# Optimization experiments

Hardware: AMD Instinct MI355X
Metric: run time of the kernel (lower is better)

Reference implementation:

```python
import jax, jax.numpy as jnp
import numpy as np

K_TOKENS = 40  # safety_token_count
LN_EPS = 1e-5


def setup_inputs() -> dict:
    key = jax.random.key(0)
    ks = jax.random.split(key, 3)
    B, S, D = 16, 4096, 768
    H = D // 2
    features = jax.random.normal(ks[0], (B, S, D), dtype=jnp.float32)
    W1 = jax.random.normal(ks[1], (D, H), dtype=jnp.float32) * (1.0 / np.sqrt(D))
    b1 = jnp.zeros((H,), dtype=jnp.float32)
    ln_gamma = jnp.ones((H,), dtype=jnp.float32)
    ln_beta = jnp.zeros((H,), dtype=jnp.float32)
    W2 = jax.random.normal(ks[2], (H, 1), dtype=jnp.float32) * (1.0 / np.sqrt(H))
    b2 = jnp.zeros((1,), dtype=jnp.float32)
    return {"features": features, "W1": W1, "b1": b1,
            "ln_gamma": ln_gamma, "ln_beta": ln_beta, "W2": W2, "b2": b2}


def _scores(features, W1, b1, ln_gamma, ln_beta, W2, b2):
    # Linear -> LayerNorm -> GELU(exact) -> Dropout(eval=identity) -> Linear -> Sigmoid
    h = jnp.einsum('bsd,dh->bsh', features, W1) + b1
    mu = jnp.mean(h, axis=-1, keepdims=True)
    var = jnp.mean(jnp.square(h - mu), axis=-1, keepdims=True)
    h = (h - mu) * jax.lax.rsqrt(var + LN_EPS) * ln_gamma + ln_beta
    h = jax.nn.gelu(h, approximate=False)
    s = jnp.einsum('bsh,ho->bso', h, W2) + b2  # [B, S, 1]
    return jax.nn.sigmoid(s[..., 0])           # [B, S]


def reference(features, W1, b1, ln_gamma, ln_beta, W2, b2):
    scores = _scores(features, W1, b1, ln_gamma, ln_beta, W2, b2)
    k = min(K_TOKENS, features.shape[1])
    _, indices = jax.lax.top_k(scores, k)                      # [B, k]
    safety_tokens = jnp.take_along_axis(features, indices[:, :, None], axis=1)  # [B, k, D]
    return safety_tokens, indices
```

## Files before the change

### kernel.cpp

```cpp
#include <hip/hip_runtime.h>
#include <math.h>

#define B_   16
#define S_   4096
#define D_   768
#define H_   384
#define NTOK (B_ * S_)
#define KTOP 40
#define NTILES 24
#define KCH    24

typedef __attribute__((ext_vector_type(8))) short bf16x8;
typedef __attribute__((ext_vector_type(4))) float f32x4;

static __device__ __forceinline__ unsigned short f2bf(float x) {
    union { float f; unsigned u; } v; v.f = x;
    unsigned r = v.u + 0x7FFF + ((v.u >> 16) & 1);
    return (unsigned short)(r >> 16);
}
static __device__ __forceinline__ float bf2f(unsigned short h) {
    union { unsigned u; float f; } v; v.u = ((unsigned)h) << 16; return v.f;
}

__global__ __launch_bounds__(64) void pack_w1(const float* __restrict__ W1,
                                              unsigned short* __restrict__ bh,
                                              unsigned short* __restrict__ bl)
{
    const int nt   = blockIdx.x;
    const int ch   = blockIdx.y;
    const int lane = threadIdx.x;
    const int n    = nt * 16 + (lane & 15);
    const int k0   = ch * 32 + (lane >> 4) * 8;

    unsigned short h8[8], l8[8];
#pragma unroll
    for (int j = 0; j < 8; ++j) {
        const float v = W1[(size_t)(k0 + j) * H_ + n];
        const unsigned short h = f2bf(v);
        h8[j] = h;
        l8[j] = f2bf(v - bf2f(h));
    }
    const size_t base = ((size_t)(nt * KCH + ch) * 64 + lane) * 8;
#pragma unroll
    for (int j = 0; j < 8; ++j) { bh[base + j] = h8[j]; bl[base + j] = l8[j]; }
}

__global__ __launch_bounds__(256) void score_kernel(
    const float* __restrict__ features,
    const unsigned short* __restrict__ bh_g,
    const unsigned short* __restrict__ bl_g,
    const float* __restrict__ b1,
    const float* __restrict__ gamma,
    const float* __restrict__ beta,
    const float* __restrict__ W2,
    const float* __restrict__ b2,
    float* __restrict__ scores)
{
    __shared__ unsigned short Ah[64][40];
    __shared__ unsigned short Al[64][40];
    __shared__ float red[4][64];
    __shared__ float mu_s[64];
    __shared__ float rs_s[64];

    const int tid  = threadIdx.x;
    const int lane = tid & 63;
    const int w    = tid >> 6;
    const int base = blockIdx.x * 64;
    const int cl   = lane & 15;
    const int p    = lane >> 4;

    f32x4 acc[4][6];
#pragma unroll
    for (int m = 0; m < 4; ++m)
#pragma unroll
        for (int t = 0; t < 6; ++t) acc[m][t] = (f32x4){0.f, 0.f, 0.f, 0.f};

    const int f0 = tid, f1 = tid + 256;
    const int r0 = f0 >> 3, c0 = (f0 & 7) * 4;
    const int r1 = f1 >> 3, c1 = (f1 & 7) * 4;

    float4 p0 = *(const float4*)(features + (size_t)(base + r0) * D_ + c0);
    float4 p1 = *(const float4*)(features + (size_t)(base + r1) * D_ + c1);

    for (int c = 0; c < KCH; ++c) {
        if (c) __syncthreads();
        {
            unsigned short h0 = f2bf(p0.x), h1 = f2bf(p0.y), h2 = f2bf(p0.z), h3 = f2bf(p0.w);
            Ah[r0][c0] = h0; Ah[r0][c0+1] = h1; Ah[r0][c0+2] = h2; Ah[r0][c0+3] = h3;
            Al[r0][c0]   = f2bf(p0.x - bf2f(h0));
            Al[r0][c0+1] = f2bf(p0.y - bf2f(h1));
            Al[r0][c0+2] = f2bf(p0.z - bf2f(h2));
            Al[r0][c0+3] = f2bf(p0.w - bf2f(h3));
            unsigned short g0 = f2bf(p1.x), g1 = f2bf(p1.y), g2 = f2bf(p1.z), g3 = f2bf(p1.w);
            Ah[r1][c1] = g0; Ah[r1][c1+1] = g1; Ah[r1][c1+2] = g2; Ah[r1][c1+3] = g3;
            Al[r1][c1]   = f2bf(p1.x - bf2f(g0));
            Al[r1][c1+1] = f2bf(p1.y - bf2f(g1));
            Al[r1][c1+2] = f2bf(p1.z - bf2f(g2));
            Al[r1][c1+3] = f2bf(p1.w - bf2f(g3));
        }
        if (c + 1 < KCH) {
            const int d0 = (c + 1) * 32;
            p0 = *(const float4*)(features + (size_t)(base + r0) * D_ + d0 + c0);
            p1 = *(const float4*)(features + (size_t)(base + r1) * D_ + d0 + c1);
        }
        __syncthreads();

        bf16x8 bhf[6], blf[6];
#pragma unroll
        for (int t = 0; t < 6; ++t) {
            const size_t bb = ((size_t)((w * 6 + t) * KCH + c) * 64 + lane) * 8;
            bhf[t] = *(const bf16x8*)(bh_g + bb);
            blf[t] = *(const bf16x8*)(bl_g + bb);
        }
        bf16x8 ahf[4], alf[4];
#pragma unroll
        for (int m = 0; m < 4; ++m) {
            const int row = m * 16 + cl;
            const int k0  = p * 8;
            ahf[m] = *(const bf16x8*)&Ah[row][k0];
            alf[m] = *(const bf16x8*)&Al[row][k0];
        }
#pragma unroll
        for (int m = 0; m < 4; ++m)
#pragma unroll
            for (int t = 0; t < 6; ++t) {
                acc[m][t] = __builtin_amdgcn_mfma_f32_16x16x32_bf16(ahf[m], bhf[t], acc[m][t], 0, 0, 0);
                acc[m][t] = __builtin_amdgcn_mfma_f32_16x16x32_bf16(ahf[m], blf[t], acc[m][t], 0, 0, 0);
                acc[m][t] = __builtin_amdgcn_mfma_f32_16x16x32_bf16(alf[m], bhf[t], acc[m][t], 0, 0, 0);
            }
    }

    float b1v[6], gv[6], bev[6], w2v[6];
#pragma unroll
    for (int t = 0; t < 6; ++t) {
        const int n = (w * 6 + t) * 16 + cl;
        b1v[t] = b1[n]; gv[t] = gamma[n]; bev[t] = beta[n]; w2v[t] = W2[n];
    }
#pragma unroll
    for (int m = 0; m < 4; ++m)
#pragma unroll
        for (int t = 0; t < 6; ++t)
#pragma unroll
            for (int r = 0; r < 4; ++r) acc[m][t][r] += b1v[t];

#pragma unroll
    for (int m = 0; m < 4; ++m) {
        float sm[4] = {0.f, 0.f, 0.f, 0.f};
#pragma unroll
        for (int t = 0; t < 6; ++t)
#pragma unroll
            for (int r = 0; r < 4; ++r) sm[r] += acc[m][t][r];
#pragma unroll
        for (int r = 0; r < 4; ++r) {
#pragma unroll
            for (int off = 1; off <= 8; off <<= 1) sm[r] += __shfl_xor(sm[r], off, 64);
        }
        if (cl == 0) {
#pragma unroll
            for (int r = 0; r < 4; ++r) red[w][m * 16 + p * 4 + r] = sm[r];
        }
    }
    __syncthreads();
    if (tid < 64) mu_s[tid] = (red[0][tid] + red[1][tid] + red[2][tid] + red[3][tid]) * (1.0f / H_);
    __syncthreads();

#pragma unroll
    for (int m = 0; m < 4; ++m) {
        float mur[4];
#pragma unroll
        for (int r = 0; r < 4; ++r) mur[r] = mu_s[m * 16 + p * 4 + r];
        float sm[4] = {0.f, 0.f, 0.f, 0.f};
#pragma unroll
        for (int t = 0; t < 6; ++t)
#pragma unroll
            for (int r = 0; r < 4; ++r) { const float d = acc[m][t][r] - mur[r]; sm[r] += d * d; }
#pragma unroll
        for (int r = 0; r < 4; ++r) {
#pragma unroll
            for (int off = 1; off <= 8; off <<= 1) sm[r] += __shfl_xor(sm[r], off, 64);
        }
        if (cl == 0) {
#pragma unroll
            for (int r = 0; r < 4; ++r) red[w][m * 16 + p * 4 + r] = sm[r];
        }
    }
    __syncthreads();
    if (tid < 64) rs_s[tid] = rsqrtf((red[0][tid] + red[1][tid] + red[2][tid] + red[3][tid]) * (1.0f / H_) + 1e-5f);
    __syncthreads();

#pragma unroll
    for (int m = 0; m < 4; ++m) {
        float mur[4], rsr[4];
#pragma unroll
        for (int r = 0; r < 4; ++r) { mur[r] = mu_s[m * 16 + p * 4 + r]; rsr[r] = rs_s[m * 16 + p * 4 + r]; }
        float sm[4] = {0.f, 0.f, 0.f, 0.f};
#pragma unroll
        for (int t = 0; t < 6; ++t)
#pragma unroll
            for (int r = 0; r < 4; ++r) {
                const float y  = (acc[m][t][r] - mur[r]) * rsr[r] * gv[t] + bev[t];
                const float ge = 0.5f * y * (1.0f + erff(y * 0.70710678118654752f));
                sm[r] = fmaf(ge, w2v[t], sm[r]);
            }
#pragma unroll
        for (int r = 0; r < 4; ++r) {
#pragma unroll
            for (int off = 1; off <= 8; off <<= 1) sm[r] += __shfl_xor(sm[r], off, 64);
        }
        if (cl == 0) {
#pragma unroll
            for (int r = 0; r < 4; ++r) red[w][m * 16 + p * 4 + r] = sm[r];
        }
    }
    __syncthreads();
    if (tid < 64) {
        const float s = red[0][tid] + red[1][tid] + red[2][tid] + red[3][tid] + b2[0];
        scores[base + tid] = 1.0f / (1.0f + expf(-s));
    }
}

__global__ __launch_bounds__(256) void select_kernel(const float* __restrict__ scores,
                                                     int* __restrict__ sel)
{
    __shared__ unsigned int bits_s[S_];
    __shared__ unsigned int hist[256];
    __shared__ int s_byte, s_above, s_rem;
    __shared__ unsigned int s_ngt, s_neq;
    __shared__ unsigned int candV[64];
    __shared__ int candI[64];
    __shared__ int eqI[256];

    const int b   = blockIdx.x;
    const int tid = threadIdx.x;

    for (int i = tid; i < S_; i += 256)
        bits_s[i] = __float_as_uint(scores[b * S_ + i]);
    if (tid == 0) { s_rem = KTOP; s_ngt = 0u; s_neq = 0u; }

    unsigned int prefix = 0u, mask = 0u;
    for (int pb = 3; pb >= 0; --pb) {
        hist[tid] = 0u;
        __syncthreads();
        for (int i = tid; i < S_; i += 256) {
            const unsigned int u = bits_s[i];
            if ((u & mask) == prefix) atomicAdd(&hist[(u >> (8 * pb)) & 255u], 1u);
        }
        __syncthreads();
        if (tid == 0) {
            int c = 0, v = 255;
            for (; v >= 0; --v) { c += (int)hist[v]; if (c >= s_rem) break; }
            s_byte  = v;
            s_above = c - (int)hist[v];
            s_rem   = s_rem - s_above;
        }
        __syncthreads();
        prefix |= ((unsigned int)s_byte) << (8 * pb);
        mask   |= 0xFFu << (8 * pb);
        __syncthreads();
    }
    const unsigned int T = prefix;
    const int need = s_rem;

    for (int i = tid; i < S_; i += 256) {
        const unsigned int u = bits_s[i];
        if (u > T) {
            const unsigned int pos = atomicAdd(&s_ngt, 1u);
            candV[pos] = u; candI[pos] = i;
        } else if (u == T) {
            const unsigned int pos = atomicAdd(&s_neq, 1u);
            if (pos < 256u) eqI[pos] = i;
        }
    }
    __syncthreads();
    const int ngt = (int)s_ngt;
    const int neq = (int)(s_neq < 256u ? s_neq : 256u);
    for (int j = tid; j < neq; j += 256) {
        int rank = 0;
        for (int l = 0; l < neq; ++l) rank += (eqI[l] < eqI[j]) ? 1 : 0;
        if (rank < need) { candV[ngt + rank] = T; candI[ngt + rank] = eqI[j]; }
    }
    __syncthreads();
    if (tid < KTOP) {
        const unsigned int u = candV[tid];
        const int idx = candI[tid];
        int rank = 0;
        for (int j = 0; j < KTOP; ++j)
            rank += (candV[j] > u || (candV[j] == u && candI[j] < idx)) ? 1 : 0;
        sel[b * KTOP + rank] = idx;
    }
}

__global__ __launch_bounds__(192) void gather_kernel(const float* __restrict__ features,
                                                     const int* __restrict__ sel,
                                                     float* __restrict__ out_tok,
                                                     float* __restrict__ out_idx)
{
    const int i = blockIdx.x;
    const int b = blockIdx.y;
    const int idx = sel[b * KTOP + i];
    const float4* src = (const float4*)(features + ((size_t)b * S_ + idx) * D_);
    float4* dst = (float4*)(out_tok + ((size_t)b * KTOP + i) * D_);
    dst[threadIdx.x] = src[threadIdx.x];
    if (threadIdx.x == 0) out_idx[b * KTOP + i] = (float)idx;
}

extern "C" void kernel_launch(void* const* d_in, const int* in_sizes, int n_in,
                              void* d_out, int out_size, void* d_ws, size_t ws_size,
                              hipStream_t stream)
{
    const float* features = (const float*)d_in[0];
    const float* W1       = (const float*)d_in[1];
    const float* b1       = (const float*)d_in[2];
    const float* gamma    = (const float*)d_in[3];
    const float* beta     = (const float*)d_in[4];
    const float* W2       = (const float*)d_in[5];
    const float* b2       = (const float*)d_in[6];

    unsigned short* bh = (unsigned short*)d_ws;
    unsigned short* bl = bh + (size_t)D_ * H_;
    float* scores      = (float*)(bl + (size_t)D_ * H_);
    int*   sel         = (int*)(scores + NTOK);

    float* out        = (float*)d_out;
    float* out_tokens = out;
    float* out_idx    = out + (size_t)B_ * KTOP * D_;

    pack_w1<<<dim3(NTILES, KCH), 64, 0, stream>>>(W1, bh, bl);
    score_kernel<<<NTOK / 64, 256, 0, stream>>>(features, bh, bl, b1, gamma, beta, W2, b2, scores);
    select_kernel<<<B_, 256, 0, stream>>>(scores, sel);
    gather_kernel<<<dim3(KTOP, B_), 192, 0, stream>>>(features, sel, out_tokens, out_idx);
}
```

Measured before the change: 510.6 us.

## Load A fragments directly from global per wave, dropping LDS staging

The shared-memory staging of the features tile is removed. Each wave now reads its MFMA A-fragments straight from global memory as float4 pairs and does the bf16 hi/lo split in registers. This drops both per-chunk __syncthreads and the LDS writes and reads. In exchange, each of the four waves in a block re-reads the same 64x32 tile, so L1/L2 traffic and VALU conversion work for A rise roughly fourfold. The explicit one-chunk prefetch is gone, replaced only by unroll 2.

```diff
diff --git a/kernel.cpp b/kernel.cpp
--- a/kernel.cpp
+++ b/kernel.cpp
@@ -56,8 +56,6 @@
     const float* __restrict__ b2,
     float* __restrict__ scores)
 {
-    __shared__ unsigned short Ah[64][40];
-    __shared__ unsigned short Al[64][40];
     __shared__ float red[4][64];
     __shared__ float mu_s[64];
     __shared__ float rs_s[64];
@@ -75,36 +73,20 @@
 #pragma unroll
         for (int t = 0; t < 6; ++t) acc[m][t] = (f32x4){0.f, 0.f, 0.f, 0.f};
 
-    const int f0 = tid, f1 = tid + 256;
-    const int r0 = f0 >> 3, c0 = (f0 & 7) * 4;
-    const int r1 = f1 >> 3, c1 = (f1 & 7) * 4;
-
-    float4 p0 = *(const float4*)(features + (size_t)(base + r0) * D_ + c0);
-    float4 p1 = *(const float4*)(features + (size_t)(base + r1) * D_ + c1);
-
+    const float* arow[4];
+#pragma unroll
+    for (int m = 0; m < 4; ++m)
+        arow[m] = features + (size_t)(base + m * 16 + cl) * D_ + p * 8;
+
+#pragma unroll 2
     for (int c = 0; c < KCH; ++c) {
-        if (c) __syncthreads();
-        {
-            unsigned short h0 = f2bf(p0.x), h1 = f2bf(p0.y), h2 = f2bf(p0.z), h3 = f2bf(p0.w);
-            Ah[r0][c0] = h0; Ah[r0][c0+1] = h1; Ah[r0][c0+2] = h2; Ah[r0][c0+3] = h3;
-            Al[r0][c0]   = f2bf(p0.x - bf2f(h0));
-            Al[r0][c0+1] = f2bf(p0.y - bf2f(h1));
-            Al[r0][c0+2] = f2bf(p0.z - bf2f(h2));
-            Al[r0][c0+3] = f2bf(p0.w - bf2f(h3));
-            unsigned short g0 = f2bf(p1.x), g1 = f2bf(p1.y), g2 = f2bf(p1.z), g3 = f2bf(p1.w);
-            Ah[r1][c1] = g0; Ah[r1][c1+1] = g1; Ah[r1][c1+2] = g2; Ah[r1][c1+3] = g3;
-            Al[r1][c1]   = f2bf(p1.x - bf2f(g0));
-            Al[r1][c1+1] = f2bf(p1.y - bf2f(g1));
-            Al[r1][c1+2] = f2bf(p1.z - bf2f(g2));
-            Al[r1][c1+3] = f2bf(p1.w - bf2f(g3));
-        }
-        if (c + 1 < KCH) {
-            const int d0 = (c + 1) * 32;
-            p0 = *(const float4*)(features + (size_t)(base + r0) * D_ + d0 + c0);
-            p1 = *(const float4*)(features + (size_t)(base + r1) * D_ + d0 + c1);
-        }
-        __syncthreads();
-
+        float4 araw0[4], araw1[4];
+#pragma unroll
+        for (int m = 0; m < 4; ++m) {
+            const float* src = arow[m] + c * 32;
+            araw0[m] = *(const float4*)(src);
+            araw1[m] = *(const float4*)(src + 4);
+        }
         bf16x8 bhf[6], blf[6];
 #pragma unroll
         for (int t = 0; t < 6; ++t) {
@@ -115,10 +97,16 @@
         bf16x8 ahf[4], alf[4];
 #pragma unroll
         for (int m = 0; m < 4; ++m) {
-            const int row = m * 16 + cl;
-            const int k0  = p * 8;
-            ahf[m] = *(const bf16x8*)&Ah[row][k0];
-            alf[m] = *(const bf16x8*)&Al[row][k0];
+            float f[8] = {araw0[m].x, araw0[m].y, araw0[m].z, araw0[m].w,
+                          araw1[m].x, araw1[m].y, araw1[m].z, araw1[m].w};
+            bf16x8 hv, lv;
+#pragma unroll
+            for (int j = 0; j < 8; ++j) {
+                const unsigned short hh = f2bf(f[j]);
+                hv[j] = (short)hh;
+                lv[j] = (short)f2bf(f[j] - bf2f(hh));
+            }
+            ahf[m] = hv; alf[m] = lv;
         }
 #pragma unroll
         for (int m = 0; m < 4; ++m)
```

Measured after the change: 646.7 us. 1.27x slower.
